# Kernel tuning notes

Measured on AMD Instinct MI355X. Metric: run time of the kernel, lower is better.

Reference implementation:

```python
import jax, jax.numpy as jnp
import numpy as np

N = 16384   # nodes
E = 262144  # edges (avg degree 16)
H = 256     # hidden_dim
R = 32      # num_radial


def _lin(k, fi, fo):
    return jax.random.normal(k, (fi, fo), jnp.float32) / np.float32(np.sqrt(fi))


def setup_inputs() -> dict:
    key = jax.random.key(0)
    ks = jax.random.split(key, 16)
    h = jax.random.normal(ks[0], (N, H), jnp.float32)
    pos = jax.random.normal(ks[1], (N, 3), jnp.float32)
    edge_index = jax.random.randint(ks[2], (2, E), 0, N, dtype=jnp.int32)
    return {
        'h': h, 'pos': pos,
        # radial_basis: Linear(1,R), SiLU, Linear(R,R)
        'rb_w1': _lin(ks[3], 1, R), 'rb_b1': jnp.zeros((R,), jnp.float32),
        'rb_w2': _lin(ks[4], R, R), 'rb_b2': jnp.zeros((R,), jnp.float32),
        # edge_network: Linear(2H+R,H), SiLU, Linear(H,H), LayerNorm(H)
        'en_w1': _lin(ks[5], 2 * H + R, H), 'en_b1': jnp.zeros((H,), jnp.float32),
        'en_w2': _lin(ks[6], H, H), 'en_b2': jnp.zeros((H,), jnp.float32),
        'en_g': jnp.ones((H,), jnp.float32), 'en_bt': jnp.zeros((H,), jnp.float32),
        # node_network: Linear(2H,H), SiLU, Linear(H,H), LayerNorm(H)
        'nn_w1': _lin(ks[7], 2 * H, H), 'nn_b1': jnp.zeros((H,), jnp.float32),
        'nn_w2': _lin(ks[8], H, H), 'nn_b2': jnp.zeros((H,), jnp.float32),
        'nn_g': jnp.ones((H,), jnp.float32), 'nn_bt': jnp.zeros((H,), jnp.float32),
        # coord_network: Linear(H,H//2), SiLU, Linear(H//2,1), Tanh
        'cn_w1': _lin(ks[9], H, H // 2), 'cn_b1': jnp.zeros((H // 2,), jnp.float32),
        'cn_w2': _lin(ks[10], H // 2, 1), 'cn_b2': jnp.zeros((1,), jnp.float32),
        'edge_index': edge_index,
    }


def _ln(x, g, b, eps=1e-5):
    mu = jnp.mean(x, axis=-1, keepdims=True)
    var = jnp.var(x, axis=-1, keepdims=True)
    return (x - mu) / jnp.sqrt(var + eps) * g + b


def reference(h, pos, rb_w1, rb_b1, rb_w2, rb_b2,
              en_w1, en_b1, en_w2, en_b2, en_g, en_bt,
              nn_w1, nn_b1, nn_w2, nn_b2, nn_g, nn_bt,
              cn_w1, cn_b1, cn_w2, cn_b2, edge_index):
    row, col = edge_index[0], edge_index[1]
    rel_pos = pos[col] - pos[row]                                   # [E,3]
    # torch: norm(rel_pos + 1e-8) -> scalar eps added to the vector first
    dist = jnp.linalg.norm(rel_pos + 1e-8, axis=-1, keepdims=True)  # [E,1]
    radial = jax.nn.silu(dist @ rb_w1 + rb_b1) @ rb_w2 + rb_b2      # [E,R]
    edge_feat = jnp.concatenate([h[row], h[col], radial], axis=-1)  # [E,2H+R]
    edge_msg = _ln(jax.nn.silu(edge_feat @ en_w1 + en_b1) @ en_w2 + en_b2,
                   en_g, en_bt)                                     # [E,H]
    # PyG propagate with aggr='add': sum messages at target nodes (col)
    node_msg = jax.ops.segment_sum(edge_msg, col, num_segments=h.shape[0])
    hn_in = jnp.concatenate([h, node_msg], axis=-1)                 # [N,2H]
    h_updated = _ln(jax.nn.silu(hn_in @ nn_w1 + nn_b1) @ nn_w2 + nn_b2,
                    nn_g, nn_bt)                                    # [N,H]
    coord_w = jnp.tanh(jax.nn.silu(edge_msg @ cn_w1 + cn_b1) @ cn_w2 + cn_b2)  # [E,1]
    weighted = rel_pos * coord_w                                    # [E,3]
    pos_updates = jnp.zeros_like(pos).at[row].add(-weighted).at[col].add(weighted)
    return h_updated, pos_updates
```

## Files before the change

kernel.cpp:

```cpp
#include <hip/hip_runtime.h>
#include <hip/hip_bf16.h>


#define NN 16384
#define EE 262144
#define HH 256
#define RR 32

typedef __bf16 bf16x8 __attribute__((ext_vector_type(8)));
typedef float f32x4 __attribute__((ext_vector_type(4)));

__device__ __forceinline__ float silu_f(float x) { return x / (1.0f + __expf(-x)); }

__device__ __forceinline__ unsigned short bf_bits(float x) {
  union { __hip_bfloat16 b; unsigned short u; } v;
  v.b = __float2bfloat16(x);
  return v.u;
}
__device__ __forceinline__ float ubf(unsigned short u) {
  return __uint_as_float(((unsigned)u) << 16);
}

__global__ __launch_bounds__(256) void conv_h_kernel(const float* __restrict__ src,
                                                     __hip_bfloat16* __restrict__ dst,
                                                     int n4) {
  int i = blockIdx.x * 256 + threadIdx.x;
  if (i >= n4) return;
  float4 v = ((const float4*)src)[i];
  __hip_bfloat16* d = dst + (size_t)i * 4;
  d[0] = __float2bfloat16(v.x);
  d[1] = __float2bfloat16(v.y);
  d[2] = __float2bfloat16(v.z);
  d[3] = __float2bfloat16(v.w);
}

__global__ __launch_bounds__(256) void tr_kernel(const float* __restrict__ in,
                                                 __hip_bfloat16* __restrict__ out,
                                                 int K, int Nc) {
  int i = blockIdx.x * 256 + threadIdx.x;
  if (i >= K * Nc) return;
  int k = i / Nc, c = i - k * Nc;
  out[(size_t)c * K + k] = __float2bfloat16(in[i]);
}

__global__ __launch_bounds__(256) void rwt_kernel(const float* __restrict__ rb_w2,
                                                  const float* __restrict__ en_w1,
                                                  __hip_bfloat16* __restrict__ RWT) {
  int t = blockIdx.x * 256 + threadIdx.x;
  if (t >= 256 * 32) return;
  int c = t >> 5, i = t & 31;
  float s = 0.f;
#pragma unroll
  for (int j = 0; j < 32; ++j) s += rb_w2[i * 32 + j] * en_w1[(512 + j) * 256 + c];
  RWT[c * 32 + i] = __float2bfloat16(s);
}

__global__ __launch_bounds__(256) void b1p_kernel(const float* __restrict__ en_b1,
                                                  const float* __restrict__ rb_b2,
                                                  const float* __restrict__ en_w1,
                                                  float* __restrict__ b1p) {
  int c = blockIdx.x * 256 + threadIdx.x;
  if (c >= 256) return;
  float s = en_b1[c];
#pragma unroll
  for (int j = 0; j < 32; ++j) s += rb_b2[j] * en_w1[(512 + j) * 256 + c];
  b1p[c] = s;
}

__global__ __launch_bounds__(256) void count_kernel(const int* __restrict__ ei,
                                                    int* __restrict__ counts) {
  int e = blockIdx.x * 256 + threadIdx.x;
  if (e >= EE) return;
  atomicAdd(&counts[ei[EE + e]], 1);
}

__global__ __launch_bounds__(256) void scanA_kernel(const int* __restrict__ counts,
                                                    int* __restrict__ bsum) {
  __shared__ int ws[4];
  int t = threadIdx.x;
  int v = counts[blockIdx.x * 256 + t];
#pragma unroll
  for (int m = 1; m < 64; m <<= 1) v += __shfl_xor(v, m, 64);
  if ((t & 63) == 0) ws[t >> 6] = v;
  __syncthreads();
  if (t == 0) bsum[blockIdx.x] = ws[0] + ws[1] + ws[2] + ws[3];
}

__global__ __launch_bounds__(64) void scanB_kernel(const int* __restrict__ bsum,
                                                   int* __restrict__ bbase,
                                                   int* __restrict__ offs) {
  int t = threadIdx.x;
  int v = bsum[t], x = v;
#pragma unroll
  for (int d = 1; d < 64; d <<= 1) {
    int y = __shfl_up(x, d, 64);
    if (t >= d) x += y;
  }
  bbase[t] = x - v;
  if (t == 63) offs[NN] = x;
}

__global__ __launch_bounds__(256) void scanC_kernel(const int* __restrict__ counts,
                                                    const int* __restrict__ bbase,
                                                    int* __restrict__ offs,
                                                    int* __restrict__ cursor) {
  __shared__ int wtot[4];
  int t = threadIdx.x, wv = t >> 6, ln = t & 63;
  int base = blockIdx.x * 256;
  int v = counts[base + t], x = v;
#pragma unroll
  for (int d = 1; d < 64; d <<= 1) {
    int y = __shfl_up(x, d, 64);
    if (ln >= d) x += y;
  }
  if (ln == 63) wtot[wv] = x;
  __syncthreads();
  int add = bbase[blockIdx.x];
  for (int k = 0; k < wv; ++k) add += wtot[k];
  int excl = add + x - v;
  offs[base + t] = excl;
  cursor[base + t] = excl;
}

__global__ __launch_bounds__(256) void scatter_kernel(const int* __restrict__ ei,
                                                      int* __restrict__ cursor,
                                                      int* __restrict__ elist) {
  int e = blockIdx.x * 256 + threadIdx.x;
  if (e >= EE) return;
  int c = ei[EE + e];
  int p = atomicAdd(&cursor[c], 1);
  elist[p] = e;
}

__global__ __launch_bounds__(512) void pgemm_kernel(const __hip_bfloat16* __restrict__ A,
                                                    const __hip_bfloat16* __restrict__ BT,
                                                    __hip_bfloat16* __restrict__ out) {
  const int tid = threadIdx.x, w = tid >> 6, l = tid & 63, r = l & 15, g = l >> 4;
  const int n0 = blockIdx.x * 64;
  f32x4 acc[4][4];
#pragma unroll
  for (int a = 0; a < 4; ++a)
#pragma unroll
    for (int b = 0; b < 4; ++b) acc[a][b] = (f32x4){0.f, 0.f, 0.f, 0.f};
  for (int ks = 0; ks < 8; ++ks) {
    bf16x8 af[4], bfr[4];
#pragma unroll
    for (int fm = 0; fm < 4; ++fm)
      af[fm] = *(const bf16x8*)(A + (size_t)(n0 + fm * 16 + r) * 256 + ks * 32 + g * 8);
#pragma unroll
    for (int fn = 0; fn < 4; ++fn)
      bfr[fn] = *(const bf16x8*)(BT + (size_t)(w * 64 + fn * 16 + r) * 256 + ks * 32 + g * 8);
#pragma unroll
    for (int fm = 0; fm < 4; ++fm)
#pragma unroll
      for (int fn = 0; fn < 4; ++fn)
        acc[fm][fn] =
            __builtin_amdgcn_mfma_f32_16x16x32_bf16(af[fm], bfr[fn], acc[fm][fn], 0, 0, 0);
  }
#pragma unroll
  for (int fm = 0; fm < 4; ++fm)
#pragma unroll
    for (int fn = 0; fn < 4; ++fn) {
      int col = w * 64 + fn * 16 + r;
#pragma unroll
      for (int q = 0; q < 4; ++q) {
        int row = n0 + fm * 16 + g * 4 + q;
        out[(size_t)row * 512 + col] = __float2bfloat16(acc[fm][fn][q]);
      }
    }
}

__global__ __launch_bounds__(512, 4) void edge_kernel(
    const __hip_bfloat16* __restrict__ Pb, const int* __restrict__ ei,
    const float* __restrict__ pos, const float* __restrict__ rb_w1,
    const float* __restrict__ rb_b1, const __hip_bfloat16* __restrict__ RWT,
    const float* __restrict__ b1p, const __hip_bfloat16* __restrict__ W2T,
    const float* __restrict__ en_b2, const float* __restrict__ en_g,
    const float* __restrict__ en_bt, const __hip_bfloat16* __restrict__ CW1T,
    const float* __restrict__ cn_b1, const float* __restrict__ cn_w2,
    const float* __restrict__ cn_b2, __hip_bfloat16* __restrict__ emsg,
    float* __restrict__ pos_out) {
  __shared__ __align__(16) __hip_bfloat16 A2[64 * 264];
  __shared__ float relb[64][3];
  __shared__ int srow[64], scol[64];
  __shared__ float red[8][64], redsq[8][64];
  __shared__ float mv[64][2];
  __shared__ float gb[HH], btb[HH], cb1b[128], cw2b[128];

  const int tid = threadIdx.x, w = tid >> 6, l = tid & 63, r = l & 15, g = l >> 4;
  const int e0 = blockIdx.x * 64;
  const int chalf = w >> 2;

  const int eloc = (w & 3) * 16 + r;
  const int eg = e0 + eloc;
  const int nr = ei[eg], nc = ei[EE + eg];
  float dx = pos[nc * 3 + 0] - pos[nr * 3 + 0] + 1e-8f;
  float dy = pos[nc * 3 + 1] - pos[nr * 3 + 1] + 1e-8f;
  float dz = pos[nc * 3 + 2] - pos[nr * 3 + 2] + 1e-8f;
  float d = sqrtf(dx * dx + dy * dy + dz * dz);
  bf16x8 sfrag;
#pragma unroll
  for (int j = 0; j < 8; ++j) {
    float x = d * rb_w1[g * 8 + j] + rb_b1[g * 8 + j];
    sfrag[j] = (__bf16)silu_f(x);
  }

  if (tid < 256) {
    gb[tid] = en_g[tid];
    btb[tid] = en_bt[tid];
  }
  if (tid < 128) {
    cb1b[tid] = cn_b1[tid];
    cw2b[tid] = cn_w2[tid];
  }
  if (tid < 64) {
    int e = e0 + tid;
    int r2 = ei[e], c2 = ei[EE + e];
    srow[tid] = r2;
    scol[tid] = c2;
    relb[tid][0] = pos[c2 * 3 + 0] - pos[r2 * 3 + 0];
    relb[tid][1] = pos[c2 * 3 + 1] - pos[r2 * 3 + 1];
    relb[tid][2] = pos[c2 * 3 + 2] - pos[r2 * 3 + 2];
  }

  const unsigned short* Pu = (const unsigned short*)Pb;
  unsigned short* A2u = (unsigned short*)A2;
#pragma unroll
  for (int t = 0; t < 8; ++t) {
    int cblk = chalf * 8 + t;
    int cbase = cblk * 16 + g * 4;
    bf16x8 afr = *(const bf16x8*)(RWT + (size_t)(cblk * 16 + r) * 32 + g * 8);
    f32x4 rad = __builtin_amdgcn_mfma_f32_16x16x32_bf16(afr, sfrag,
                                                        (f32x4){0.f, 0.f, 0.f, 0.f}, 0, 0, 0);
    ushort4 p1 = *(const ushort4*)(Pu + (size_t)nr * 512 + cbase);
    ushort4 p2 = *(const ushort4*)(Pu + (size_t)nc * 512 + 256 + cbase);
    float4 b1v = *(const float4*)(b1p + cbase);
    ushort4 o;
    o.x = bf_bits(silu_f(rad[0] + ubf(p1.x) + ubf(p2.x) + b1v.x));
    o.y = bf_bits(silu_f(rad[1] + ubf(p1.y) + ubf(p2.y) + b1v.y));
    o.z = bf_bits(silu_f(rad[2] + ubf(p1.z) + ubf(p2.z) + b1v.z));
    o.w = bf_bits(silu_f(rad[3] + ubf(p1.w) + ubf(p2.w) + b1v.w));
    *(ushort4*)(A2u + (size_t)eloc * 264 + cbase) = o;
  }
  __syncthreads();

  f32x4 acc[4][2];
#pragma unroll
  for (int a = 0; a < 4; ++a)
#pragma unroll
    for (int b = 0; b < 2; ++b) acc[a][b] = (f32x4){0.f, 0.f, 0.f, 0.f};
  for (int ks = 0; ks < 8; ++ks) {
    bf16x8 af[4], bfr[2];
#pragma unroll
    for (int fm = 0; fm < 4; ++fm)
      af[fm] = *(const bf16x8*)(A2 + (fm * 16 + r) * 264 + ks * 32 + g * 8);
#pragma unroll
    for (int fn = 0; fn < 2; ++fn)
      bfr[fn] = *(const bf16x8*)(W2T + (size_t)(w * 32 + fn * 16 + r) * 256 + ks * 32 + g * 8);
#pragma unroll
    for (int fm = 0; fm < 4; ++fm)
#pragma unroll
      for (int fn = 0; fn < 2; ++fn)
        acc[fm][fn] =
            __builtin_amdgcn_mfma_f32_16x16x32_bf16(af[fm], bfr[fn], acc[fm][fn], 0, 0, 0);
  }
#pragma unroll
  for (int fn = 0; fn < 2; ++fn) {
    float b2 = en_b2[w * 32 + fn * 16 + r];
#pragma unroll
    for (int fm = 0; fm < 4; ++fm)
#pragma unroll
      for (int q = 0; q < 4; ++q) acc[fm][fn][q] += b2;
  }

#pragma unroll
  for (int fm = 0; fm < 4; ++fm)
#pragma unroll
    for (int q = 0; q < 4; ++q) {
      float s = acc[fm][0][q] + acc[fm][1][q];
      float sq = acc[fm][0][q] * acc[fm][0][q] + acc[fm][1][q] * acc[fm][1][q];
#pragma unroll
      for (int m = 1; m < 16; m <<= 1) {
        s += __shfl_xor(s, m, 64);
        sq += __shfl_xor(sq, m, 64);
      }
      if (r == 0) {
        red[w][fm * 16 + g * 4 + q] = s;
        redsq[w][fm * 16 + g * 4 + q] = sq;
      }
    }
  __syncthreads();
  if (tid < 64) {
    float s = 0.f, sq = 0.f;
#pragma unroll
    for (int k = 0; k < 8; ++k) {
      s += red[k][tid];
      sq += redsq[k][tid];
    }
    float mean = s * (1.0f / HH);
    float var = sq * (1.0f / HH) - mean * mean;
    mv[tid][0] = mean;
    mv[tid][1] = rsqrtf(var + 1e-5f);
  }
  __syncthreads();
#pragma unroll
  for (int fn = 0; fn < 2; ++fn) {
    int col = w * 32 + fn * 16 + r;
    float gg = gb[col], bb = btb[col];
#pragma unroll
    for (int fm = 0; fm < 4; ++fm)
#pragma unroll
      for (int q = 0; q < 4; ++q) {
        int row = fm * 16 + g * 4 + q;
        A2[row * 264 + col] =
            __float2bfloat16((acc[fm][fn][q] - mv[row][0]) * mv[row][1] * gg + bb);
      }
  }
  __syncthreads();

#pragma unroll
  for (int it = 0; it < 4; ++it) {
    int ch = it * 512 + tid;
    int i = ch >> 5, c = ch & 31;
    *(float4*)(emsg + (size_t)(e0 + i) * HH + c * 8) = *(const float4*)(A2 + i * 264 + c * 8);
  }

  f32x4 c2a[4];
#pragma unroll
  for (int a = 0; a < 4; ++a) c2a[a] = (f32x4){0.f, 0.f, 0.f, 0.f};
  for (int ks = 0; ks < 8; ++ks) {
    bf16x8 af[4];
#pragma unroll
    for (int fm = 0; fm < 4; ++fm)
      af[fm] = *(const bf16x8*)(A2 + (fm * 16 + r) * 264 + ks * 32 + g * 8);
    bf16x8 bfr = *(const bf16x8*)(CW1T + (size_t)(w * 16 + r) * 256 + ks * 32 + g * 8);
#pragma unroll
    for (int fm = 0; fm < 4; ++fm)
      c2a[fm] = __builtin_amdgcn_mfma_f32_16x16x32_bf16(af[fm], bfr, c2a[fm], 0, 0, 0);
  }
  {
    int ccol = w * 16 + r;
    float cb = cb1b[ccol], cw = cw2b[ccol];
#pragma unroll
    for (int fm = 0; fm < 4; ++fm)
#pragma unroll
      for (int q = 0; q < 4; ++q) {
        float v = silu_f(c2a[fm][q] + cb) * cw;
#pragma unroll
        for (int m = 1; m < 16; m <<= 1) v += __shfl_xor(v, m, 64);
        if (r == 0) red[w][fm * 16 + g * 4 + q] = v;
      }
  }
  __syncthreads();
  if (tid < 64) {
    float s = cn_b2[0];
#pragma unroll
    for (int k = 0; k < 8; ++k) s += red[k][tid];
    float wgt = tanhf(s);
    float ax = relb[tid][0], ay = relb[tid][1], az = relb[tid][2];
    int rr = srow[tid], cc = scol[tid];
    atomicAdd(&pos_out[rr * 3 + 0], -wgt * ax);
    atomicAdd(&pos_out[rr * 3 + 1], -wgt * ay);
    atomicAdd(&pos_out[rr * 3 + 2], -wgt * az);
    atomicAdd(&pos_out[cc * 3 + 0], wgt * ax);
    atomicAdd(&pos_out[cc * 3 + 1], wgt * ay);
    atomicAdd(&pos_out[cc * 3 + 2], wgt * az);
  }
}

__global__ __launch_bounds__(256) void nodemsg_kernel(const int* __restrict__ offs,
                                                      const int* __restrict__ elist,
                                                      const __hip_bfloat16* __restrict__ emsg,
                                                      __hip_bfloat16* __restrict__ nmsgb) {
  int wid = threadIdx.x >> 6, l = threadIdx.x & 63;
  int n = blockIdx.x * 4 + wid;
  float a0 = 0.f, a1 = 0.f, a2 = 0.f, a3 = 0.f;
  int b = offs[n], e2 = offs[n + 1];
  const unsigned short* E = (const unsigned short*)emsg;
  int idx = b;
  for (; idx + 1 < e2; idx += 2) {
    int ea = elist[idx], eb = elist[idx + 1];
    ushort4 va = *(const ushort4*)(E + (size_t)ea * HH + l * 4);
    ushort4 vb = *(const ushort4*)(E + (size_t)eb * HH + l * 4);
    a0 += ubf(va.x) + ubf(vb.x);
    a1 += ubf(va.y) + ubf(vb.y);
    a2 += ubf(va.z) + ubf(vb.z);
    a3 += ubf(va.w) + ubf(vb.w);
  }
  if (idx < e2) {
    int ea = elist[idx];
    ushort4 va = *(const ushort4*)(E + (size_t)ea * HH + l * 4);
    a0 += ubf(va.x);
    a1 += ubf(va.y);
    a2 += ubf(va.z);
    a3 += ubf(va.w);
  }
  ushort4 o;
  o.x = bf_bits(a0);
  o.y = bf_bits(a1);
  o.z = bf_bits(a2);
  o.w = bf_bits(a3);
  *(ushort4*)((unsigned short*)nmsgb + (size_t)n * HH + l * 4) = o;
}

__global__ __launch_bounds__(512, 4) void node_kernel(
    const __hip_bfloat16* __restrict__ hb, const __hip_bfloat16* __restrict__ nmsgb,
    const __hip_bfloat16* __restrict__ NW1T, const float* __restrict__ nn_b1,
    const __hip_bfloat16* __restrict__ NW2T, const float* __restrict__ nn_b2,
    const float* __restrict__ nn_g, const float* __restrict__ nn_bt,
    float* __restrict__ out_h) {
  __shared__ __align__(16) __hip_bfloat16 A2[32 * 264];
  __shared__ float red[8][32], redsq[8][32];
  __shared__ float mv[32][2];
  __shared__ float gb[HH], btb[HH];
  const int tid = threadIdx.x, w = tid >> 6, l = tid & 63, r = l & 15, g = l >> 4;
  const int n0 = blockIdx.x * 32;
  if (tid < 256) {
    gb[tid] = nn_g[tid];
    btb[tid] = nn_bt[tid];
  }

  f32x4 acc[2][2];
#pragma unroll
  for (int a = 0; a < 2; ++a)
#pragma unroll
    for (int b = 0; b < 2; ++b) acc[a][b] = (f32x4){0.f, 0.f, 0.f, 0.f};
  for (int ks = 0; ks < 8; ++ks) {
    bf16x8 af[2], bfr[2];
#pragma unroll
    for (int fm = 0; fm < 2; ++fm)
      af[fm] = *(const bf16x8*)(hb + (size_t)(n0 + fm * 16 + r) * 256 + ks * 32 + g * 8);
#pragma unroll
    for (int fn = 0; fn < 2; ++fn)
      bfr[fn] = *(const bf16x8*)(NW1T + (size_t)(w * 32 + fn * 16 + r) * 512 + ks * 32 + g * 8);
#pragma unroll
    for (int fm = 0; fm < 2; ++fm)
#pragma unroll
      for (int fn = 0; fn < 2; ++fn)
        acc[fm][fn] =
            __builtin_amdgcn_mfma_f32_16x16x32_bf16(af[fm], bfr[fn], acc[fm][fn], 0, 0, 0);
  }
  for (int ks = 0; ks < 8; ++ks) {
    bf16x8 af[2], bfr[2];
#pragma unroll
    for (int fm = 0; fm < 2; ++fm)
      af[fm] = *(const bf16x8*)(nmsgb + (size_t)(n0 + fm * 16 + r) * 256 + ks * 32 + g * 8);
#pragma unroll
    for (int fn = 0; fn < 2; ++fn)
      bfr[fn] =
          *(const bf16x8*)(NW1T + (size_t)(w * 32 + fn * 16 + r) * 512 + 256 + ks * 32 + g * 8);
#pragma unroll
    for (int fm = 0; fm < 2; ++fm)
#pragma unroll
      for (int fn = 0; fn < 2; ++fn)
        acc[fm][fn] =
            __builtin_amdgcn_mfma_f32_16x16x32_bf16(af[fm], bfr[fn], acc[fm][fn], 0, 0, 0);
  }
  __syncthreads();
#pragma unroll
  for (int fn = 0; fn < 2; ++fn) {
    int col = w * 32 + fn * 16 + r;
    float b1 = nn_b1[col];
#pragma unroll
    for (int fm = 0; fm < 2; ++fm)
#pragma unroll
      for (int q = 0; q < 4; ++q) {
        int row = fm * 16 + g * 4 + q;
        A2[row * 264 + col] = __float2bfloat16(silu_f(acc[fm][fn][q] + b1));
      }
  }
  __syncthreads();

#pragma unroll
  for (int a = 0; a < 2; ++a)
#pragma unroll
    for (int b = 0; b < 2; ++b) acc[a][b] = (f32x4){0.f, 0.f, 0.f, 0.f};
  for (int ks = 0; ks < 8; ++ks) {
    bf16x8 af[2], bfr[2];
#pragma unroll
    for (int fm = 0; fm < 2; ++fm)
      af[fm] = *(const bf16x8*)(A2 + (fm * 16 + r) * 264 + ks * 32 + g * 8);
#pragma unroll
    for (int fn = 0; fn < 2; ++fn)
      bfr[fn] = *(const bf16x8*)(NW2T + (size_t)(w * 32 + fn * 16 + r) * 256 + ks * 32 + g * 8);
#pragma unroll
    for (int fm = 0; fm < 2; ++fm)
#pragma unroll
      for (int fn = 0; fn < 2; ++fn)
        acc[fm][fn] =
            __builtin_amdgcn_mfma_f32_16x16x32_bf16(af[fm], bfr[fn], acc[fm][fn], 0, 0, 0);
  }
#pragma unroll
  for (int fn = 0; fn < 2; ++fn) {
    float b2 = nn_b2[w * 32 + fn * 16 + r];
#pragma unroll
    for (int fm = 0; fm < 2; ++fm)
#pragma unroll
      for (int q = 0; q < 4; ++q) acc[fm][fn][q] += b2;
  }
#pragma unroll
  for (int fm = 0; fm < 2; ++fm)
#pragma unroll
    for (int q = 0; q < 4; ++q) {
      float s = acc[fm][0][q] + acc[fm][1][q];
      float sq = acc[fm][0][q] * acc[fm][0][q] + acc[fm][1][q] * acc[fm][1][q];
#pragma unroll
      for (int m = 1; m < 16; m <<= 1) {
        s += __shfl_xor(s, m, 64);
        sq += __shfl_xor(sq, m, 64);
      }
      if (r == 0) {
        red[w][fm * 16 + g * 4 + q] = s;
        redsq[w][fm * 16 + g * 4 + q] = sq;
      }
    }
  __syncthreads();
  if (tid < 32) {
    float s = 0.f, sq = 0.f;
#pragma unroll
    for (int k = 0; k < 8; ++k) {
      s += red[k][tid];
      sq += redsq[k][tid];
    }
    float mean = s * (1.0f / HH);
    float var = sq * (1.0f / HH) - mean * mean;
    mv[tid][0] = mean;
    mv[tid][1] = rsqrtf(var + 1e-5f);
  }
  __syncthreads();
#pragma unroll
  for (int fn = 0; fn < 2; ++fn) {
    int col = w * 32 + fn * 16 + r;
    float gg = gb[col], bb = btb[col];
#pragma unroll
    for (int fm = 0; fm < 2; ++fm)
#pragma unroll
      for (int q = 0; q < 4; ++q) {
        int row = fm * 16 + g * 4 + q;
        out_h[(size_t)(n0 + row) * HH + col] =
            (acc[fm][fn][q] - mv[row][0]) * mv[row][1] * gg + bb;
      }
  }
}

extern "C" void kernel_launch(void* const* d_in, const int* in_sizes, int n_in,
                              void* d_out, int out_size, void* d_ws, size_t ws_size,
                              hipStream_t stream) {
  const float* h = (const float*)d_in[0];
  const float* pos = (const float*)d_in[1];
  const float* rb_w1 = (const float*)d_in[2];
  const float* rb_b1 = (const float*)d_in[3];
  const float* rb_w2 = (const float*)d_in[4];
  const float* rb_b2 = (const float*)d_in[5];
  const float* en_w1 = (const float*)d_in[6];
  const float* en_b1 = (const float*)d_in[7];
  const float* en_w2 = (const float*)d_in[8];
  const float* en_b2 = (const float*)d_in[9];
  const float* en_g = (const float*)d_in[10];
  const float* en_bt = (const float*)d_in[11];
  const float* nn_w1 = (const float*)d_in[12];
  const float* nn_b1 = (const float*)d_in[13];
  const float* nn_w2 = (const float*)d_in[14];
  const float* nn_b2 = (const float*)d_in[15];
  const float* nn_g = (const float*)d_in[16];
  const float* nn_bt = (const float*)d_in[17];
  const float* cn_w1 = (const float*)d_in[18];
  const float* cn_b1 = (const float*)d_in[19];
  const float* cn_w2 = (const float*)d_in[20];
  const float* cn_b2 = (const float*)d_in[21];
  const int* ei = (const int*)d_in[22];

  float* out_h = (float*)d_out;
  float* out_pos = out_h + (size_t)NN * HH;

  char* p = (char*)d_ws;
  auto alloc = [&p](size_t bytes) {
    char* q = p;
    p += (bytes + 255) & ~(size_t)255;
    return q;
  };
  __hip_bfloat16* hb = (__hip_bfloat16*)alloc((size_t)NN * HH * 2);
  __hip_bfloat16* Pb = (__hip_bfloat16*)alloc((size_t)NN * 512 * 2);
  __hip_bfloat16* W1abT = (__hip_bfloat16*)alloc((size_t)512 * 256 * 2);
  __hip_bfloat16* W2T = (__hip_bfloat16*)alloc((size_t)256 * 256 * 2);
  __hip_bfloat16* NW1T = (__hip_bfloat16*)alloc((size_t)256 * 512 * 2);
  __hip_bfloat16* NW2T = (__hip_bfloat16*)alloc((size_t)256 * 256 * 2);
  __hip_bfloat16* CW1T = (__hip_bfloat16*)alloc((size_t)128 * 256 * 2);
  __hip_bfloat16* RWT = (__hip_bfloat16*)alloc((size_t)256 * 32 * 2);
  float* b1p = (float*)alloc((size_t)256 * 4);
  __hip_bfloat16* emsg = (__hip_bfloat16*)alloc((size_t)EE * HH * 2);
  __hip_bfloat16* nmsgb = (__hip_bfloat16*)alloc((size_t)NN * HH * 2);
  int* counts = (int*)alloc((size_t)NN * 4);
  int* offs = (int*)alloc((size_t)(NN + 1) * 4);
  int* cursor = (int*)alloc((size_t)NN * 4);
  int* elist = (int*)alloc((size_t)EE * 4);
  int* bsum = (int*)alloc((size_t)64 * 4);
  int* bbase = (int*)alloc((size_t)64 * 4);

  hipMemsetAsync(out_pos, 0, (size_t)NN * 3 * sizeof(float), stream);
  hipMemsetAsync(counts, 0, (size_t)NN * sizeof(int), stream);

  conv_h_kernel<<<(NN * HH / 4 + 255) / 256, 256, 0, stream>>>(h, hb, NN * HH / 4);
  tr_kernel<<<(256 * 256) / 256, 256, 0, stream>>>(en_w2, W2T, 256, 256);
  tr_kernel<<<(512 * 256) / 256, 256, 0, stream>>>(nn_w1, NW1T, 512, 256);
  tr_kernel<<<(256 * 256) / 256, 256, 0, stream>>>(nn_w2, NW2T, 256, 256);
  tr_kernel<<<(256 * 128) / 256, 256, 0, stream>>>(cn_w1, CW1T, 256, 128);
  tr_kernel<<<(256 * 256) / 256, 256, 0, stream>>>(en_w1, W1abT, 256, 256);
  tr_kernel<<<(256 * 256) / 256, 256, 0, stream>>>(en_w1 + 256 * 256, W1abT + 256 * 256, 256,
                                                   256);
  rwt_kernel<<<(256 * 32) / 256, 256, 0, stream>>>(rb_w2, en_w1, RWT);
  b1p_kernel<<<1, 256, 0, stream>>>(en_b1, rb_b2, en_w1, b1p);
  count_kernel<<<EE / 256, 256, 0, stream>>>(ei, counts);
  scanA_kernel<<<NN / 256, 256, 0, stream>>>(counts, bsum);
  scanB_kernel<<<1, 64, 0, stream>>>(bsum, bbase, offs);
  scanC_kernel<<<NN / 256, 256, 0, stream>>>(counts, bbase, offs, cursor);
  scatter_kernel<<<EE / 256, 256, 0, stream>>>(ei, cursor, elist);
  pgemm_kernel<<<NN / 64, 512, 0, stream>>>(hb, W1abT, Pb);
  edge_kernel<<<EE / 64, 512, 0, stream>>>(Pb, ei, pos, rb_w1, rb_b1, RWT, b1p, W2T, en_b2,
                                           en_g, en_bt, CW1T, cn_b1, cn_w2, cn_b2, emsg,
                                           out_pos);
  nodemsg_kernel<<<NN / 4, 256, 0, stream>>>(offs, elist, emsg, nmsgb);
  node_kernel<<<NN / 32, 512, 0, stream>>>(hb, nmsgb, NW1T, nn_b1, NW2T, nn_b2, nn_g, nn_bt,
                                           out_h);
}
```

Before: 521.4 us.

## Process edges in col-sorted order so segment sum reads contiguous messages

The edge kernel now processes edges in the CSR order given by elist, so each node's incoming messages are written contiguously and the node-message reduction reads them sequentially without indirection. The first-layer gather of Pb rows is moved into a separate vectorised pass over LDS using shared row/col indices. The second GEMM is transposed (weights as A operand, edges as B) so LayerNorm reductions need fewer shuffles and writes are vectorised. The cost is an extra LDS pass and sync, plus gathers of ei and pos through elist, which lose some coalescing.

Result: no change. 513.0 us (-1.6%).

```diff
diff --git a/kernel.cpp b/kernel.cpp
--- a/kernel.cpp
+++ b/kernel.cpp
@@ -178,117 +178,141 @@
     const float* __restrict__ en_b2, const float* __restrict__ en_g,
     const float* __restrict__ en_bt, const __hip_bfloat16* __restrict__ CW1T,
     const float* __restrict__ cn_b1, const float* __restrict__ cn_w2,
-    const float* __restrict__ cn_b2, __hip_bfloat16* __restrict__ emsg,
-    float* __restrict__ pos_out) {
+    const float* __restrict__ cn_b2, const int* __restrict__ elist,
+    __hip_bfloat16* __restrict__ emsg, float* __restrict__ pos_out) {
   __shared__ __align__(16) __hip_bfloat16 A2[64 * 264];
   __shared__ float relb[64][3];
+  __shared__ float distb[64];
   __shared__ int srow[64], scol[64];
   __shared__ float red[8][64], redsq[8][64];
   __shared__ float mv[64][2];
-  __shared__ float gb[HH], btb[HH], cb1b[128], cw2b[128];
+  __shared__ float cb1b[128], cw2b[128];
 
   const int tid = threadIdx.x, w = tid >> 6, l = tid & 63, r = l & 15, g = l >> 4;
   const int e0 = blockIdx.x * 64;
-  const int chalf = w >> 2;
-
-  const int eloc = (w & 3) * 16 + r;
-  const int eg = e0 + eloc;
-  const int nr = ei[eg], nc = ei[EE + eg];
-  float dx = pos[nc * 3 + 0] - pos[nr * 3 + 0] + 1e-8f;
-  float dy = pos[nc * 3 + 1] - pos[nr * 3 + 1] + 1e-8f;
-  float dz = pos[nc * 3 + 2] - pos[nr * 3 + 2] + 1e-8f;
-  float d = sqrtf(dx * dx + dy * dy + dz * dz);
-  bf16x8 sfrag;
-#pragma unroll
-  for (int j = 0; j < 8; ++j) {
-    float x = d * rb_w1[g * 8 + j] + rb_b1[g * 8 + j];
-    sfrag[j] = (__bf16)silu_f(x);
-  }
-
-  if (tid < 256) {
-    gb[tid] = en_g[tid];
-    btb[tid] = en_bt[tid];
-  }
+
   if (tid < 128) {
     cb1b[tid] = cn_b1[tid];
     cw2b[tid] = cn_w2[tid];
   }
   if (tid < 64) {
-    int e = e0 + tid;
+    int e = elist[e0 + tid];
     int r2 = ei[e], c2 = ei[EE + e];
     srow[tid] = r2;
     scol[tid] = c2;
-    relb[tid][0] = pos[c2 * 3 + 0] - pos[r2 * 3 + 0];
-    relb[tid][1] = pos[c2 * 3 + 1] - pos[r2 * 3 + 1];
-    relb[tid][2] = pos[c2 * 3 + 2] - pos[r2 * 3 + 2];
-  }
-
-  const unsigned short* Pu = (const unsigned short*)Pb;
+    float dx = pos[c2 * 3 + 0] - pos[r2 * 3 + 0];
+    float dy = pos[c2 * 3 + 1] - pos[r2 * 3 + 1];
+    float dz = pos[c2 * 3 + 2] - pos[r2 * 3 + 2];
+    relb[tid][0] = dx;
+    relb[tid][1] = dy;
+    relb[tid][2] = dz;
+    float ex = dx + 1e-8f, ey = dy + 1e-8f, ez = dz + 1e-8f;
+    distb[tid] = sqrtf(ex * ex + ey * ey + ez * ez);
+  }
+  __syncthreads();
+
   unsigned short* A2u = (unsigned short*)A2;
-#pragma unroll
-  for (int t = 0; t < 8; ++t) {
-    int cblk = chalf * 8 + t;
-    int cbase = cblk * 16 + g * 4;
-    bf16x8 afr = *(const bf16x8*)(RWT + (size_t)(cblk * 16 + r) * 32 + g * 8);
-    f32x4 rad = __builtin_amdgcn_mfma_f32_16x16x32_bf16(afr, sfrag,
-                                                        (f32x4){0.f, 0.f, 0.f, 0.f}, 0, 0, 0);
-    ushort4 p1 = *(const ushort4*)(Pu + (size_t)nr * 512 + cbase);
-    ushort4 p2 = *(const ushort4*)(Pu + (size_t)nc * 512 + 256 + cbase);
-    float4 b1v = *(const float4*)(b1p + cbase);
-    ushort4 o;
-    o.x = bf_bits(silu_f(rad[0] + ubf(p1.x) + ubf(p2.x) + b1v.x));
-    o.y = bf_bits(silu_f(rad[1] + ubf(p1.y) + ubf(p2.y) + b1v.y));
-    o.z = bf_bits(silu_f(rad[2] + ubf(p1.z) + ubf(p2.z) + b1v.z));
-    o.w = bf_bits(silu_f(rad[3] + ubf(p1.w) + ubf(p2.w) + b1v.w));
-    *(ushort4*)(A2u + (size_t)eloc * 264 + cbase) = o;
-  }
-  __syncthreads();
-
-  f32x4 acc[4][2];
-#pragma unroll
-  for (int a = 0; a < 4; ++a)
-#pragma unroll
-    for (int b = 0; b < 2; ++b) acc[a][b] = (f32x4){0.f, 0.f, 0.f, 0.f};
+  {
+    const int eloc = (w & 3) * 16 + r;
+    const int chalf = w >> 2;
+    float d = distb[eloc];
+    bf16x8 sfrag;
+#pragma unroll
+    for (int j = 0; j < 8; ++j) {
+      float x = d * rb_w1[g * 8 + j] + rb_b1[g * 8 + j];
+      sfrag[j] = (__bf16)silu_f(x);
+    }
+#pragma unroll
+    for (int t = 0; t < 8; ++t) {
+      int cblk = chalf * 8 + t;
+      int cbase = cblk * 16 + g * 4;
+      bf16x8 afr = *(const bf16x8*)(RWT + (size_t)(cblk * 16 + r) * 32 + g * 8);
+      f32x4 rad = __builtin_amdgcn_mfma_f32_16x16x32_bf16(
+          afr, sfrag, (f32x4){0.f, 0.f, 0.f, 0.f}, 0, 0, 0);
+      ushort4 o;
+      o.x = bf_bits(rad[0]);
+      o.y = bf_bits(rad[1]);
+      o.z = bf_bits(rad[2]);
+      o.w = bf_bits(rad[3]);
+      *(ushort4*)(A2u + (size_t)eloc * 264 + cbase) = o;
+    }
+  }
+  __syncthreads();
+
+#pragma unroll
+  for (int it = 0; it < 4; ++it) {
+    int ch = it * 512 + tid;
+    int i = ch >> 5, c = ch & 31;
+    bf16x8 radv = *(const bf16x8*)(A2 + i * 264 + c * 8);
+    bf16x8 p1 = *(const bf16x8*)(Pb + (size_t)srow[i] * 512 + c * 8);
+    bf16x8 p2 = *(const bf16x8*)(Pb + (size_t)scol[i] * 512 + 256 + c * 8);
+    float4 b1a = *(const float4*)(b1p + c * 8);
+    float4 b1b = *(const float4*)(b1p + c * 8 + 4);
+    float bv[8] = {b1a.x, b1a.y, b1a.z, b1a.w, b1b.x, b1b.y, b1b.z, b1b.w};
+    bf16x8 o;
+#pragma unroll
+    for (int j = 0; j < 8; ++j)
+      o[j] = (__bf16)silu_f((float)radv[j] + (float)p1[j] + (float)p2[j] + bv[j]);
+    *(bf16x8*)(A2 + i * 264 + c * 8) = o;
+  }
+  __syncthreads();
+
+  f32x4 acc[2][4];
+#pragma unroll
+  for (int a = 0; a < 2; ++a)
+#pragma unroll
+    for (int b = 0; b < 4; ++b) acc[a][b] = (f32x4){0.f, 0.f, 0.f, 0.f};
   for (int ks = 0; ks < 8; ++ks) {
-    bf16x8 af[4], bfr[2];
-#pragma unroll
-    for (int fm = 0; fm < 4; ++fm)
-      af[fm] = *(const bf16x8*)(A2 + (fm * 16 + r) * 264 + ks * 32 + g * 8);
-#pragma unroll
-    for (int fn = 0; fn < 2; ++fn)
-      bfr[fn] = *(const bf16x8*)(W2T + (size_t)(w * 32 + fn * 16 + r) * 256 + ks * 32 + g * 8);
-#pragma unroll
-    for (int fm = 0; fm < 4; ++fm)
-#pragma unroll
-      for (int fn = 0; fn < 2; ++fn)
-        acc[fm][fn] =
-            __builtin_amdgcn_mfma_f32_16x16x32_bf16(af[fm], bfr[fn], acc[fm][fn], 0, 0, 0);
-  }
-#pragma unroll
-  for (int fn = 0; fn < 2; ++fn) {
-    float b2 = en_b2[w * 32 + fn * 16 + r];
-#pragma unroll
-    for (int fm = 0; fm < 4; ++fm)
-#pragma unroll
-      for (int q = 0; q < 4; ++q) acc[fm][fn][q] += b2;
-  }
-
-#pragma unroll
-  for (int fm = 0; fm < 4; ++fm)
-#pragma unroll
-    for (int q = 0; q < 4; ++q) {
-      float s = acc[fm][0][q] + acc[fm][1][q];
-      float sq = acc[fm][0][q] * acc[fm][0][q] + acc[fm][1][q] * acc[fm][1][q];
-#pragma unroll
-      for (int m = 1; m < 16; m <<= 1) {
-        s += __shfl_xor(s, m, 64);
-        sq += __shfl_xor(sq, m, 64);
+    bf16x8 af[2], bfr[4];
+#pragma unroll
+    for (int mf = 0; mf < 2; ++mf)
+      af[mf] = *(const bf16x8*)(W2T + (size_t)(w * 32 + mf * 16 + r) * 256 + ks * 32 + g * 8);
+#pragma unroll
+    for (int nf = 0; nf < 4; ++nf)
+      bfr[nf] = *(const bf16x8*)(A2 + (nf * 16 + r) * 264 + ks * 32 + g * 8);
+#pragma unroll
+    for (int mf = 0; mf < 2; ++mf)
+#pragma unroll
+      for (int nf = 0; nf < 4; ++nf)
+        acc[mf][nf] =
+            __builtin_amdgcn_mfma_f32_16x16x32_bf16(af[mf], bfr[nf], acc[mf][nf], 0, 0, 0);
+  }
+  {
+    float4 b2v0 = *(const float4*)(en_b2 + w * 32 + g * 4);
+    float4 b2v1 = *(const float4*)(en_b2 + w * 32 + 16 + g * 4);
+#pragma unroll
+    for (int nf = 0; nf < 4; ++nf) {
+      acc[0][nf][0] += b2v0.x;
+      acc[0][nf][1] += b2v0.y;
+      acc[0][nf][2] += b2v0.z;
+      acc[0][nf][3] += b2v0.w;
+      acc[1][nf][0] += b2v1.x;
+      acc[1][nf][1] += b2v1.y;
+      acc[1][nf][2] += b2v1.z;
+      acc[1][nf][3] += b2v1.w;
+    }
+  }
+
+#pragma unroll
+  for (int nf = 0; nf < 4; ++nf) {
+    float s = 0.f, sq = 0.f;
+#pragma unroll
+    for (int mf = 0; mf < 2; ++mf)
+#pragma unroll
+      for (int q = 0; q < 4; ++q) {
+        float v = acc[mf][nf][q];
+        s += v;
+        sq += v * v;
       }
-      if (r == 0) {
-        red[w][fm * 16 + g * 4 + q] = s;
-        redsq[w][fm * 16 + g * 4 + q] = sq;
-      }
-    }
+    s += __shfl_xor(s, 16, 64);
+    s += __shfl_xor(s, 32, 64);
+    sq += __shfl_xor(sq, 16, 64);
+    sq += __shfl_xor(sq, 32, 64);
+    if (l < 16) {
+      red[w][nf * 16 + l] = s;
+      redsq[w][nf * 16 + l] = sq;
+    }
+  }
   __syncthreads();
   if (tid < 64) {
     float s = 0.f, sq = 0.f;
@@ -303,18 +327,28 @@
     mv[tid][1] = rsqrtf(var + 1e-5f);
   }
   __syncthreads();
-#pragma unroll
-  for (int fn = 0; fn < 2; ++fn) {
-    int col = w * 32 + fn * 16 + r;
-    float gg = gb[col], bb = btb[col];
-#pragma unroll
-    for (int fm = 0; fm < 4; ++fm)
-#pragma unroll
-      for (int q = 0; q < 4; ++q) {
-        int row = fm * 16 + g * 4 + q;
-        A2[row * 264 + col] =
-            __float2bfloat16((acc[fm][fn][q] - mv[row][0]) * mv[row][1] * gg + bb);
-      }
+
+  {
+    float4 gv0 = *(const float4*)(en_g + w * 32 + g * 4);
+    float4 gv1 = *(const float4*)(en_g + w * 32 + 16 + g * 4);
+    float4 bv0 = *(const float4*)(en_bt + w * 32 + g * 4);
+    float4 bv1 = *(const float4*)(en_bt + w * 32 + 16 + g * 4);
+#pragma unroll
+    for (int nf = 0; nf < 4; ++nf) {
+      int e = nf * 16 + r;
+      float mm = mv[e][0], rs = mv[e][1];
+      ushort4 o0, o1;
+      o0.x = bf_bits((acc[0][nf][0] - mm) * rs * gv0.x + bv0.x);
+      o0.y = bf_bits((acc[0][nf][1] - mm) * rs * gv0.y + bv0.y);
+      o0.z = bf_bits((acc[0][nf][2] - mm) * rs * gv0.z + bv0.z);
+      o0.w = bf_bits((acc[0][nf][3] - mm) * rs * gv0.w + bv0.w);
+      o1.x = bf_bits((acc[1][nf][0] - mm) * rs * gv1.x + bv1.x);
+      o1.y = bf_bits((acc[1][nf][1] - mm) * rs * gv1.y + bv1.y);
+      o1.z = bf_bits((acc[1][nf][2] - mm) * rs * gv1.z + bv1.z);
+      o1.w = bf_bits((acc[1][nf][3] - mm) * rs * gv1.w + bv1.w);
+      *(ushort4*)(A2u + (size_t)e * 264 + w * 32 + g * 4) = o0;
+      *(ushort4*)(A2u + (size_t)e * 264 + w * 32 + 16 + g * 4) = o1;
+    }
   }
   __syncthreads();
 
@@ -369,7 +403,6 @@
 }
 
 __global__ __launch_bounds__(256) void nodemsg_kernel(const int* __restrict__ offs,
-                                                      const int* __restrict__ elist,
                                                       const __hip_bfloat16* __restrict__ emsg,
                                                       __hip_bfloat16* __restrict__ nmsgb) {
   int wid = threadIdx.x >> 6, l = threadIdx.x & 63;
@@ -377,19 +410,17 @@
   float a0 = 0.f, a1 = 0.f, a2 = 0.f, a3 = 0.f;
   int b = offs[n], e2 = offs[n + 1];
   const unsigned short* E = (const unsigned short*)emsg;
-  int idx = b;
-  for (; idx + 1 < e2; idx += 2) {
-    int ea = elist[idx], eb = elist[idx + 1];
-    ushort4 va = *(const ushort4*)(E + (size_t)ea * HH + l * 4);
-    ushort4 vb = *(const ushort4*)(E + (size_t)eb * HH + l * 4);
+  int p = b;
+  for (; p + 1 < e2; p += 2) {
+    ushort4 va = *(const ushort4*)(E + (size_t)p * HH + l * 4);
+    ushort4 vb = *(const ushort4*)(E + (size_t)(p + 1) * HH + l * 4);
     a0 += ubf(va.x) + ubf(vb.x);
     a1 += ubf(va.y) + ubf(vb.y);
     a2 += ubf(va.z) + ubf(vb.z);
     a3 += ubf(va.w) + ubf(vb.w);
   }
-  if (idx < e2) {
-    int ea = elist[idx];
-    ushort4 va = *(const ushort4*)(E + (size_t)ea * HH + l * 4);
+  if (p < e2) {
+    ushort4 va = *(const ushort4*)(E + (size_t)p * HH + l * 4);
     a0 += ubf(va.x);
     a1 += ubf(va.y);
     a2 += ubf(va.z);
@@ -617,9 +648,9 @@
   scatter_kernel<<<EE / 256, 256, 0, stream>>>(ei, cursor, elist);
   pgemm_kernel<<<NN / 64, 512, 0, stream>>>(hb, W1abT, Pb);
   edge_kernel<<<EE / 64, 512, 0, stream>>>(Pb, ei, pos, rb_w1, rb_b1, RWT, b1p, W2T, en_b2,
-                                           en_g, en_bt, CW1T, cn_b1, cn_w2, cn_b2, emsg,
-                                           out_pos);
-  nodemsg_kernel<<<NN / 4, 256, 0, stream>>>(offs, elist, emsg, nmsgb);
+                                           en_g, en_bt, CW1T, cn_b1, cn_w2, cn_b2, elist,
+                                           emsg, out_pos);
+  nodemsg_kernel<<<NN / 4, 256, 0, stream>>>(offs, emsg, nmsgb);
   node_kernel<<<NN / 32, 512, 0, stream>>>(hb, nmsgb, NW1T, nn_b1, NW2T, nn_b2, nn_g, nn_bt,
                                            out_h);
 }
```
